# Kernel tuning notes

Hardware: AMD Instinct MI355X
Metric: run time of the kernel (lower is better)

## Reference

```python
import itertools
import jax, jax.numpy as jnp
import numpy as np

N_SLOTS = 8  # = n_parts (square assignment, so Hungarian == optimal permutation)
PERMS = jnp.asarray(list(itertools.permutations(range(N_SLOTS))), dtype=jnp.int32)  # (8!, 8)
ROWS = jnp.arange(N_SLOTS)[None, :]  # (1, 8)
LOG_CLAMP = -100.0  # torch F.binary_cross_entropy clamps log terms at -100
EPS = 1e-4


def setup_inputs() -> dict:
    key = jax.random.key(0)
    k1, k2, k3, k4 = jax.random.split(key, 4)
    B, S, N, A = 16, N_SLOTS, 131072, 18
    # pred seg mask holds log-probabilities (torch.exp is applied before BCE)
    pred_seg_logp = jnp.log(jax.random.uniform(k1, (B, S, N), minval=EPS, maxval=1.0 - EPS))
    # pred affordance holds probabilities (fed to BCE directly)
    pred_aff = jax.random.uniform(k2, (B, S, A), minval=EPS, maxval=1.0 - EPS)
    gt_seg_mask = jax.random.randint(k3, (B, N), 0, S, dtype=jnp.int32)
    gt_aff = jax.random.randint(k4, (B, S, A), 0, 2, dtype=jnp.int32)
    return {"pred_seg_logp": pred_seg_logp, "pred_aff": pred_aff,
            "gt_seg_mask": gt_seg_mask, "gt_aff": gt_aff}


def _bce_cost_matrix(log_p, log_1mp, g):
    # cost[b,i,j] = mean_k BCE(p[b,i,k], g[b,j,k]); g is binary {0,1}
    # = -( sum_k g[b,j,k]*log_p[b,i,k] + sum_k (1-g[b,j,k])*log_1mp[b,i,k] ) / K
    K = log_p.shape[-1]
    t1 = jnp.einsum('bik,bjk->bij', log_p, g)
    t2 = jnp.einsum('bik,bjk->bij', log_1mp, 1.0 - g)
    return -(t1 + t2) / K


def _min_assignment_loss(cost):
    # cost: (B, S, S). Optimal assignment via brute force over permutations
    # (equivalent to linear_sum_assignment for square matrices), then
    # sum of matched costs averaged over batch.
    pc = cost[:, ROWS, PERMS].sum(-1)  # (B, 8!)
    return jnp.min(pc, axis=1).mean()


def reference(pred_seg_logp, pred_aff, gt_seg_mask, gt_aff):
    B, S, N = pred_seg_logp.shape
    # one-hot gt parts: (B, n_parts, N)
    g_seg = (gt_seg_mask[:, None, :] == jnp.arange(S)[None, :, None]).astype(jnp.float32)
    # BCE(exp(logp), g): log(p) = logp, log(1-p) = log1p(-exp(logp)), both clamped
    lgp = jnp.maximum(pred_seg_logp, LOG_CLAMP)
    lg1m = jnp.maximum(jnp.log1p(-jnp.exp(pred_seg_logp)), LOG_CLAMP)
    seg_cost = _bce_cost_matrix(lgp, lg1m, g_seg)  # (B, S, S)
    seg_loss = _min_assignment_loss(seg_cost)

    g_aff = gt_aff.astype(jnp.float32)
    lgp_a = jnp.maximum(jnp.log(pred_aff), LOG_CLAMP)
    lg1m_a = jnp.maximum(jnp.log1p(-pred_aff), LOG_CLAMP)
    aff_cost = _bce_cost_matrix(lgp_a, lg1m_a, g_aff)  # (B, S, S)
    aff_loss = _min_assignment_loss(aff_cost)

    loss = aff_loss + 3.0 * seg_loss
    return jnp.stack([seg_loss, aff_loss, loss])
```

## Files before the change

kernel.cpp:

```cpp
#include <hip/hip_runtime.h>

#define NB 16
#define NS 8
#define NPTS 131072
#define NA 18

#define THREADS 256
#define WAVES (THREADS / 64)
#define CHUNKS 64
#define ELEMS (NPTS / CHUNKS)
#define PT_PER_WAVE (ELEMS / WAVES)
#define ITERS (PT_PER_WAVE / 32)

#define PARTIALS 72
#define WS_RES (NB * CHUNKS * PARTIALS)

__device__ __forceinline__ void proc_elem(float x, int m, float acc[8], float& tsum) {
    float lgp  = fmaxf(x, -100.0f);
    float e    = __expf(x);
    float lg1m = fmaxf(__logf(1.0f - e), -100.0f);
    float d    = lgp - lg1m;
    tsum += lg1m;
#pragma unroll
    for (int j = 0; j < 8; ++j) acc[j] += (m == j) ? d : 0.0f;
}

__global__ __launch_bounds__(THREADS) void seg_accum_kernel(
    const float* __restrict__ logp, const int* __restrict__ mask,
    float* __restrict__ ws) {
    const int chunk = blockIdx.x;
    const int b = blockIdx.y;
    const int tid = (int)threadIdx.x;
    const int wave = tid >> 6;
    const int lane = tid & 63;
    const int g = lane >> 3;
    const int t = lane & 7;

    const int ptbase = chunk * ELEMS + wave * PT_PER_WAVE;
    const int4*   m4  = (const int4*)(mask + (size_t)b * NPTS + ptbase);
    const float4* lp4 = (const float4*)(logp + ((size_t)(b * NS + g)) * NPTS + ptbase);

    float acc[8] = {0.f, 0.f, 0.f, 0.f, 0.f, 0.f, 0.f, 0.f};
    float ts = 0.f;

#pragma unroll
    for (int it = 0; it < ITERS; ++it) {
        const int idx = it * 8 + t;
        const int4   mm = m4[idx];
        const float4 lp = lp4[idx];
        proc_elem(lp.x, mm.x, acc, ts);
        proc_elem(lp.y, mm.y, acc, ts);
        proc_elem(lp.z, mm.z, acc, ts);
        proc_elem(lp.w, mm.w, acc, ts);
    }

#pragma unroll
    for (int off = 4; off > 0; off >>= 1) {
#pragma unroll
        for (int j = 0; j < 8; ++j) acc[j] += __shfl_down(acc[j], off);
        ts += __shfl_down(ts, off);
    }

    __shared__ float red[WAVES][NS][9];
    if (t == 0) {
#pragma unroll
        for (int j = 0; j < 8; ++j) red[wave][g][j] = acc[j];
        red[wave][g][8] = ts;
    }
    __syncthreads();

    if (tid < PARTIALS) {
        const int gg = tid / 9, jj = tid % 9;
        float v = red[0][gg][jj] + red[1][gg][jj] + red[2][gg][jj] + red[3][gg][jj];
        ws[((size_t)(b * CHUNKS + chunk)) * PARTIALS + tid] = v;
    }
}

__global__ __launch_bounds__(64) void assign_kernel(
    const float* __restrict__ parts, const float* __restrict__ pred_aff,
    const int* __restrict__ gt_aff, float* __restrict__ res) {
    const int bw = blockIdx.x;
    const int b = bw >> 1;
    const int w = bw & 1;
    const int lane = (int)threadIdx.x;
    const int i = lane >> 3, j = lane & 7;

    __shared__ float cost[8][8];
    __shared__ float dp[256];

    float c;
    if (w == 0) {
        float sp = 0.f, tt = 0.f;
        for (int cch = 0; cch < CHUNKS; ++cch) {
            const float* p = parts + ((size_t)(b * CHUNKS + cch)) * PARTIALS;
            sp += p[i * 9 + j];
            tt += p[i * 9 + 8];
        }
        c = -(sp + tt) * (1.0f / (float)NPTS);
    } else {
        float a = 0.f;
#pragma unroll
        for (int k = 0; k < NA; ++k) {
            float p = pred_aff[((b * NS + i) * NA) + k];
            float g = (float)gt_aff[((b * NS + j) * NA) + k];
            float lgp = fmaxf(__logf(p), -100.0f);
            float l1m = fmaxf(__logf(1.0f - p), -100.0f);
            a += g * lgp + (1.0f - g) * l1m;
        }
        c = -a * (1.0f / (float)NA);
    }
    cost[i][j] = c;

    dp[lane] = 1e30f; dp[lane + 64] = 1e30f; dp[lane + 128] = 1e30f; dp[lane + 192] = 1e30f;
    __syncthreads();
    if (lane == 0) dp[0] = 0.f;
    __syncthreads();

    for (int l = 1; l <= 8; ++l) {
#pragma unroll
        for (int base = 0; base < 256; base += 64) {
            const int mm = base + lane;
            if (__popc(mm) == l) {
                float best = 1e30f;
#pragma unroll
                for (int jj = 0; jj < 8; ++jj) {
                    if (mm & (1 << jj))
                        best = fminf(best, dp[mm ^ (1 << jj)] + cost[l - 1][jj]);
                }
                dp[mm] = best;
            }
        }
        __syncthreads();
    }
    if (lane == 0) res[bw] = dp[255];
}

__global__ __launch_bounds__(64) void writeout_kernel(
    const float* __restrict__ res, float* __restrict__ out) {
    const int lane = (int)threadIdx.x;
    float v = (lane < 2 * NB) ? res[lane] : 0.f;
    float segv = ((lane & 1) == 0) ? v : 0.f;
    float affv = ((lane & 1) == 1) ? v : 0.f;
#pragma unroll
    for (int off = 32; off > 0; off >>= 1) {
        segv += __shfl_down(segv, off);
        affv += __shfl_down(affv, off);
    }
    if (lane == 0) {
        const float seg = segv * (1.0f / (float)NB);
        const float aff = affv * (1.0f / (float)NB);
        out[0] = seg;
        out[1] = aff;
        out[2] = aff + 3.0f * seg;
    }
}

extern "C" void kernel_launch(void* const* d_in, const int* in_sizes, int n_in,
                              void* d_out, int out_size, void* d_ws, size_t ws_size,
                              hipStream_t stream) {
    const float* pred_seg_logp = (const float*)d_in[0];
    const float* pred_aff      = (const float*)d_in[1];
    const int*   gt_seg_mask   = (const int*)d_in[2];
    const int*   gt_aff        = (const int*)d_in[3];
    float* out = (float*)d_out;
    float* ws  = (float*)d_ws;

    dim3 grid(CHUNKS, NB);
    seg_accum_kernel<<<grid, THREADS, 0, stream>>>(pred_seg_logp, gt_seg_mask, ws);
    assign_kernel<<<NB * 2, 64, 0, stream>>>(ws, pred_aff, gt_aff, ws + WS_RES);
    writeout_kernel<<<1, 64, 0, stream>>>(ws + WS_RES, out);
}
```

Baseline: 124.8 us.

## Fuse seg accumulation, assignment DP and writeout into one last-block kernel

Merges the three launches into one kernel. Each block writes its partial sums, then bumps a global atomic counter, and only the last block to arrive reduces all partials, builds both cost matrices, runs the subset DP and writes the output. The partials layout is transposed so the final reduction can read contiguous float4 values per entry. This removes two kernel launches and their gaps, but serializes the 32 assignment DPs inside one block. It also relies on the workspace counter starting at a fixed poison value, which the kernel resets afterwards.

```diff
diff --git a/kernel.cpp b/kernel.cpp
--- a/kernel.cpp
+++ b/kernel.cpp
@@ -6,14 +6,16 @@
 #define NA 18
 
 #define THREADS 256
-#define WAVES (THREADS / 64)
+#define WAVES 4
 #define CHUNKS 64
+#define GRID (NB * CHUNKS)
 #define ELEMS (NPTS / CHUNKS)
 #define PT_PER_WAVE (ELEMS / WAVES)
 #define ITERS (PT_PER_WAVE / 32)
 
 #define PARTIALS 72
-#define WS_RES (NB * CHUNKS * PARTIALS)
+#define WS_CTR (NB * PARTIALS * CHUNKS)
+#define POISON 0xAAAAAAAAu
 
 __device__ __forceinline__ void proc_elem(float x, int m, float acc[8], float& tsum) {
     float lgp  = fmaxf(x, -100.0f);
@@ -25,11 +27,12 @@
     for (int j = 0; j < 8; ++j) acc[j] += (m == j) ? d : 0.0f;
 }
 
-__global__ __launch_bounds__(THREADS) void seg_accum_kernel(
+__global__ __launch_bounds__(THREADS, 4) void fused_loss_kernel(
     const float* __restrict__ logp, const int* __restrict__ mask,
-    float* __restrict__ ws) {
-    const int chunk = blockIdx.x;
-    const int b = blockIdx.y;
+    const float* __restrict__ pred_aff, const int* __restrict__ gt_aff,
+    float* __restrict__ ws, float* __restrict__ out) {
+    const int chunk = blockIdx.x & (CHUNKS - 1);
+    const int b = blockIdx.x >> 6;
     const int tid = (int)threadIdx.x;
     const int wave = tid >> 6;
     const int lane = tid & 63;
@@ -72,86 +75,102 @@
     if (tid < PARTIALS) {
         const int gg = tid / 9, jj = tid % 9;
         float v = red[0][gg][jj] + red[1][gg][jj] + red[2][gg][jj] + red[3][gg][jj];
-        ws[((size_t)(b * CHUNKS + chunk)) * PARTIALS + tid] = v;
+        ws[((size_t)b * PARTIALS + tid) * CHUNKS + chunk] = v;
     }
-}
+    __syncthreads();
 
-__global__ __launch_bounds__(64) void assign_kernel(
-    const float* __restrict__ parts, const float* __restrict__ pred_aff,
-    const int* __restrict__ gt_aff, float* __restrict__ res) {
-    const int bw = blockIdx.x;
-    const int b = bw >> 1;
-    const int w = bw & 1;
-    const int lane = (int)threadIdx.x;
-    const int i = lane >> 3, j = lane & 7;
+    __shared__ int isLast;
+    unsigned* ctr = (unsigned*)ws + WS_CTR;
+    if (tid == 0) {
+        __threadfence();
+        unsigned old = __hip_atomic_fetch_add(ctr, 1u, __ATOMIC_ACQ_REL,
+                                              __HIP_MEMORY_SCOPE_AGENT);
+        isLast = (old == POISON + (unsigned)(GRID - 1));
+        if (isLast)
+            __hip_atomic_store(ctr, POISON, __ATOMIC_RELAXED, __HIP_MEMORY_SCOPE_AGENT);
+    }
+    __syncthreads();
+    if (!isLast) return;
 
-    __shared__ float cost[8][8];
-    __shared__ float dp[256];
+    __shared__ float raw[NB][PARTIALS];
+    for (int idx = tid; idx < NB * PARTIALS; idx += THREADS) {
+        const int bb = idx / PARTIALS, e = idx % PARTIALS;
+        const float4* p4 = (const float4*)(ws + ((size_t)bb * PARTIALS + e) * CHUNKS);
+        float s = 0.f;
+#pragma unroll
+        for (int c4 = 0; c4 < CHUNKS / 4; ++c4) {
+            const float4 v = p4[c4];
+            s += v.x + v.y + v.z + v.w;
+        }
+        raw[bb][e] = s;
+    }
+    __syncthreads();
 
-    float c;
-    if (w == 0) {
-        float sp = 0.f, tt = 0.f;
-        for (int cch = 0; cch < CHUNKS; ++cch) {
-            const float* p = parts + ((size_t)(b * CHUNKS + cch)) * PARTIALS;
-            sp += p[i * 9 + j];
-            tt += p[i * 9 + 8];
-        }
-        c = -(sp + tt) * (1.0f / (float)NPTS);
-    } else {
+    __shared__ float cost[2 * NB][64];
+    for (int idx = tid; idx < NB * 64; idx += THREADS) {
+        const int bb = idx >> 6, ij = idx & 63, i = ij >> 3, j = ij & 7;
+        cost[bb * 2][ij] = -(raw[bb][i * 9 + j] + raw[bb][i * 9 + 8]) * (1.0f / (float)NPTS);
+    }
+    for (int idx = tid; idx < NB * 64; idx += THREADS) {
+        const int bb = idx >> 6, i = (idx >> 3) & 7, j = idx & 7;
         float a = 0.f;
 #pragma unroll
         for (int k = 0; k < NA; ++k) {
-            float p = pred_aff[((b * NS + i) * NA) + k];
-            float g = (float)gt_aff[((b * NS + j) * NA) + k];
-            float lgp = fmaxf(__logf(p), -100.0f);
-            float l1m = fmaxf(__logf(1.0f - p), -100.0f);
-            a += g * lgp + (1.0f - g) * l1m;
+            const float p = pred_aff[((bb * NS + i) * NA) + k];
+            const float gg = (float)gt_aff[((bb * NS + j) * NA) + k];
+            a += gg * fmaxf(__logf(p), -100.0f) +
+                 (1.0f - gg) * fmaxf(__logf(1.0f - p), -100.0f);
         }
-        c = -a * (1.0f / (float)NA);
+        cost[bb * 2 + 1][idx & 63] = -a * (1.0f / (float)NA);
     }
-    cost[i][j] = c;
-
-    dp[lane] = 1e30f; dp[lane + 64] = 1e30f; dp[lane + 128] = 1e30f; dp[lane + 192] = 1e30f;
-    __syncthreads();
-    if (lane == 0) dp[0] = 0.f;
     __syncthreads();
 
-    for (int l = 1; l <= 8; ++l) {
+    __shared__ float dp[WAVES][256];
+    __shared__ float res[2 * NB];
+    const int wv = wave, ln = lane;
+    for (int pr = 0; pr < 8; ++pr) {
+        const int p = wv * 8 + pr;
+        dp[wv][ln] = 1e30f; dp[wv][ln + 64] = 1e30f;
+        dp[wv][ln + 128] = 1e30f; dp[wv][ln + 192] = 1e30f;
+        __syncthreads();
+        if (ln == 0) dp[wv][0] = 0.f;
+        __syncthreads();
+        for (int l = 1; l <= 8; ++l) {
 #pragma unroll
-        for (int base = 0; base < 256; base += 64) {
-            const int mm = base + lane;
-            if (__popc(mm) == l) {
-                float best = 1e30f;
+            for (int base = 0; base < 256; base += 64) {
+                const int mm = base + ln;
+                if (__popc(mm) == l) {
+                    float best = 1e30f;
 #pragma unroll
-                for (int jj = 0; jj < 8; ++jj) {
-                    if (mm & (1 << jj))
-                        best = fminf(best, dp[mm ^ (1 << jj)] + cost[l - 1][jj]);
+                    for (int jj = 0; jj < 8; ++jj) {
+                        if (mm & (1 << jj))
+                            best = fminf(best, dp[wv][mm ^ (1 << jj)] + cost[p][(l - 1) * 8 + jj]);
+                    }
+                    dp[wv][mm] = best;
                 }
-                dp[mm] = best;
             }
+            __syncthreads();
         }
+        if (ln == 0) res[p] = dp[wv][255];
         __syncthreads();
     }
-    if (lane == 0) res[bw] = dp[255];
-}
 
-__global__ __launch_bounds__(64) void writeout_kernel(
-    const float* __restrict__ res, float* __restrict__ out) {
-    const int lane = (int)threadIdx.x;
-    float v = (lane < 2 * NB) ? res[lane] : 0.f;
-    float segv = ((lane & 1) == 0) ? v : 0.f;
-    float affv = ((lane & 1) == 1) ? v : 0.f;
+    if (wv == 0) {
+        float v = (ln < 2 * NB) ? res[ln] : 0.f;
+        float segv = ((ln & 1) == 0) ? v : 0.f;
+        float affv = ((ln & 1) == 1) ? v : 0.f;
 #pragma unroll
-    for (int off = 32; off > 0; off >>= 1) {
-        segv += __shfl_down(segv, off);
-        affv += __shfl_down(affv, off);
-    }
-    if (lane == 0) {
-        const float seg = segv * (1.0f / (float)NB);
-        const float aff = affv * (1.0f / (float)NB);
-        out[0] = seg;
-        out[1] = aff;
-        out[2] = aff + 3.0f * seg;
+        for (int off = 32; off > 0; off >>= 1) {
+            segv += __shfl_down(segv, off);
+            affv += __shfl_down(affv, off);
+        }
+        if (ln == 0) {
+            const float seg = segv * (1.0f / (float)NB);
+            const float aff = affv * (1.0f / (float)NB);
+            out[0] = seg;
+            out[1] = aff;
+            out[2] = aff + 3.0f * seg;
+        }
     }
 }
 
@@ -165,8 +184,6 @@
     float* out = (float*)d_out;
     float* ws  = (float*)d_ws;
 
-    dim3 grid(CHUNKS, NB);
-    seg_accum_kernel<<<grid, THREADS, 0, stream>>>(pred_seg_logp, gt_seg_mask, ws);
-    assign_kernel<<<NB * 2, 64, 0, stream>>>(ws, pred_aff, gt_aff, ws + WS_RES);
-    writeout_kernel<<<1, 64, 0, stream>>>(ws + WS_RES, out);
+    fused_loss_kernel<<<GRID, THREADS, 0, stream>>>(
+        pred_seg_logp, gt_seg_mask, pred_aff, gt_aff, ws, out);
 }
```

Result: slower. 252.4 us (+102.2%).
